# Kernel tuning notes

Measured on AMD Instinct MI355X. Metric: run time of the kernel, lower is better.

## Reference

```python
import jax, jax.numpy as jnp
import numpy as np

N = 50000; E = 800000; T = 800000; G = 64
H = 128; IEMB = 128; BAS = 8; NS = 4; NR = 6; OEH = 128; OUT = 1; NB = 4; CUT = 5.0


def envelope(x):
    # exponent=5 -> p=6: 1/x + a*x^5 + b*x^6 + c*x^7 with a=-28, b=48, c=-21
    return 1.0 / x - 28.0 * x**5 + 48.0 * x**6 - 21.0 * x**7


def setup_inputs() -> dict:
    key = jax.random.key(0)
    ks = iter(jax.random.split(key, 80))
    def w(shape, s=0.1):
        return jax.random.normal(next(ks), shape, dtype=jnp.float32) * s
    inp = {}
    inp['z'] = jax.random.randint(next(ks), (N,), 0, 100, dtype=jnp.int32)
    inp['dist'] = jax.random.uniform(next(ks), (E,), jnp.float32, 0.05, 1.0)
    inp['dist_trip'] = jax.random.uniform(next(ks), (T,), jnp.float32, 0.05, 1.0)
    inp['angle'] = jax.random.uniform(next(ks), (T,), jnp.float32, -1.0, 1.0)
    inp['edge_index'] = jax.random.randint(next(ks), (2, E), 0, N, dtype=jnp.int32)
    inp['triplets'] = jax.random.randint(next(ks), (T, 3), 0, N, dtype=jnp.int32)
    inp['batch'] = jnp.sort(jax.random.randint(next(ks), (N,), 0, G, dtype=jnp.int32))
    inp['atom_table'] = w((100, H), 1.0)
    inp['rbf_freq'] = jnp.arange(1, NR + 1, dtype=jnp.float32) * jnp.float32(np.pi)
    inp['sbf_freq'] = jnp.arange(1, NR + 1, dtype=jnp.float32) * jnp.float32(np.pi)
    inp['emb_w1'] = w((NR, IEMB)); inp['emb_b1'] = w((IEMB,), 0.01)
    inp['emb_w2'] = w((IEMB, H)); inp['emb_b2'] = w((H,), 0.01)
    inp['iw_rbf1'] = w((NB, NR, BAS)); inp['iw_rbf2'] = w((NB, BAS, H))
    inp['iw_sbf1'] = w((NB, NS * NR, BAS)); inp['iw_sbf2'] = w((NB, BAS, IEMB))
    inp['iw_t1'] = w((NB, H, IEMB)); inp['iw_t2'] = w((NB, IEMB, H)); inp['ib_t2'] = w((NB, H), 0.01)
    inp['iw_up'] = w((NB, H, H)); inp['ib_up'] = w((NB, H), 0.01)
    inp['iw_down'] = w((NB, H, H)); inp['ib_down'] = w((NB, H), 0.01)
    inp['ow_rbf'] = w((NB + 1, NR, H))
    inp['ow0'] = w((NB + 1, H, OEH)); inp['ob0'] = w((NB + 1, OEH), 0.01)
    inp['ow1'] = w((NB + 1, OEH, OEH)); inp['ob1'] = w((NB + 1, OEH), 0.01)
    inp['ow2'] = w((NB + 1, OEH, OUT)); inp['ob2'] = w((NB + 1, OUT), 0.01)
    return inp


def _forward(atom_table, rbf_freq, sbf_freq, emb_w1, emb_b1, emb_w2, emb_b2,
             iw_rbf1, iw_rbf2, iw_sbf1, iw_sbf2, iw_t1, iw_t2, ib_t2,
             iw_up, ib_up, iw_down, ib_down, ow_rbf, ow0, ob0, ow1, ob1, ow2, ob2,
             dist, dist_trip, angle, z, edge_index, triplets, batch):
    row, col = edge_index[0], edge_index[1]
    j_idx = triplets[:, 1]
    # radial basis for edges: [E, NR]
    d = dist[:, None] / CUT
    rbf_e = envelope(d) * jnp.sin(rbf_freq * d)
    # spherical basis for triplets: [T, NS*NR]
    dt = dist_trip[:, None] / CUT
    rbf_t = envelope(dt) * jnp.sin(sbf_freq * dt)
    a = angle[:, None]
    sph = jnp.concatenate([jnp.ones_like(a), a, 0.5 * (3 * a**2 - 1), 0.5 * (5 * a**3 - 3 * a)], axis=-1)
    sbf_t = (rbf_t[:, None, :] * sph[:, :, None]).reshape(a.shape[0], -1)

    x = atom_table[z]  # [N, H]
    # EmbeddingBlock: edge msg from rbf only, scattered to col
    e = jax.nn.silu(rbf_e @ emb_w1 + emb_b1) @ emb_w2 + emb_b2
    x = x + jax.ops.segment_sum(e, col, num_segments=N)

    def out_block(k, x):
        rbf_emb = rbf_e @ ow_rbf[k]            # [E, H]
        h = jax.ops.segment_sum(x[row] * rbf_emb, col, num_segments=N)
        h = jax.nn.silu(h @ ow0[k] + ob0[k])
        h = jax.nn.silu(h @ ow1[k] + ob1[k])
        return h @ ow2[k] + ob2[k]             # [N, OUT]

    P = out_block(0, x)
    for b in range(NB):
        x_up = x @ iw_up[b] + ib_up[b]
        x_down = x @ iw_down[b] + ib_down[b]
        rbf_emb = jax.nn.silu(rbf_e @ iw_rbf1[b]) @ iw_rbf2[b]      # [E, H]
        x_edge = x_up[row] * rbf_emb                                  # [E, H]
        sbf_emb = jax.nn.silu(sbf_t @ iw_sbf1[b]) @ iw_sbf2[b]      # [T, H]
        t = jax.nn.silu(x_down @ iw_t1[b]) @ iw_t2[b] + ib_t2[b]     # [N, H]
        # original: for each triplet i, x_edge += t[j]*sbf_emb[i] (broadcast over all edges)
        extra = jnp.sum(t[j_idx] * sbf_emb, axis=0)                   # [H]
        x_edge = x_edge + extra
        x = x + jax.ops.segment_sum(x_edge, col, num_segments=N)
        P = P + out_block(b + 1, x)

    counts = jax.ops.segment_sum(jnp.ones((x.shape[0],), jnp.float32), batch, num_segments=G)
    pooled = jax.ops.segment_sum(P, batch, num_segments=G) / jnp.maximum(counts, 1.0)[:, None]
    return pooled  # [G, OUT]


def reference(z, dist, dist_trip, angle, edge_index, triplets, batch, atom_table, rbf_freq, sbf_freq,
              emb_w1, emb_b1, emb_w2, emb_b2, iw_rbf1, iw_rbf2, iw_sbf1, iw_sbf2, iw_t1, iw_t2, ib_t2,
              iw_up, ib_up, iw_down, ib_down, ow_rbf, ow0, ob0, ow1, ob1, ow2, ob2):
    return _forward(atom_table, rbf_freq, sbf_freq, emb_w1, emb_b1, emb_w2, emb_b2,
                    iw_rbf1, iw_rbf2, iw_sbf1, iw_sbf2, iw_t1, iw_t2, ib_t2,
                    iw_up, ib_up, iw_down, ib_down, ow_rbf, ow0, ob0, ow1, ob1, ow2, ob2,
                    dist, dist_trip, angle, z, edge_index, triplets, batch)
```

## Files before the change

### kernel.cpp

```cpp
#include <hip/hip_runtime.h>
#include <hip/hip_fp16.h>

#define N_ 50000
#define E_ 800000
#define T_ 800000
#define G_ 64
#define H_ 128

#define NBK 782
#define NSB (NBK * 8)
#define CAPS 320

typedef __attribute__((ext_vector_type(8))) short bf16x8;
typedef __attribute__((ext_vector_type(4))) float f32x4;
typedef _Float16 f16x2 __attribute__((ext_vector_type(2)));

__device__ __forceinline__ float siluf(float v) {
    return __fdividef(v, 1.0f + __expf(-v));
}

__device__ __forceinline__ unsigned short f2bf(float f) {
    unsigned int u = __float_as_uint(f);
    u += 0x7fffu + ((u >> 16) & 1u);
    return (unsigned short)(u >> 16);
}
__device__ __forceinline__ unsigned int f2bf2(float a, float b) {
    return (unsigned int)f2bf(a) | ((unsigned int)f2bf(b) << 16);
}
__device__ __forceinline__ float bf2f(unsigned short h) {
    return __uint_as_float(((unsigned int)h) << 16);
}
__device__ __forceinline__ float2 bf2x2(unsigned int p) {
    return make_float2(__uint_as_float(p << 16), __uint_as_float(p & 0xffff0000u));
}
__device__ __forceinline__ float fdot2f(f16x2 a, f16x2 b, float c) {
    return __builtin_amdgcn_fdot2(a, b, c, false);
}

__global__ __launch_bounds__(256) void k_bucket(const int* __restrict__ ecol, const int* __restrict__ erow,
                                                const float* __restrict__ dist,
                                                const int* __restrict__ trip,
                                                const float* __restrict__ dist_trip, const float* __restrict__ angle,
                                                int* bcntE, int4* __restrict__ ebkt,
                                                int* bcntT, int4* __restrict__ tbkt) {
    int i = blockIdx.x * 256 + threadIdx.x;
    int r = blockIdx.x & 7;
    if (i < E_) {
        int col = ecol[i];
        int sb = (col >> 6) * 8 + r;
        int pos = atomicAdd(&bcntE[sb], 1);
        if (pos < CAPS)
            ebkt[(size_t)sb * CAPS + pos] = make_int4(erow[i], __float_as_int(dist[i]), col & 63, 0);
    }
    int t = i - E_;
    if (t >= 0 && t < T_) {
        int j = trip[3 * t + 1];
        int sb = (j >> 6) * 8 + r;
        int pos = atomicAdd(&bcntT[sb], 1);
        if (pos < CAPS)
            tbkt[(size_t)sb * CAPS + pos] = make_int4(__float_as_int(dist_trip[t]), __float_as_int(angle[t]), j & 63, 0);
    }
}

__global__ __launch_bounds__(256) void k_cnt(const int* __restrict__ bcntE, const int4* __restrict__ ebkt,
                                             const int* __restrict__ bcntT, const int4* __restrict__ tbkt,
                                             int* __restrict__ degE, int* __restrict__ degT) {
    int b = blockIdx.x;
    bool isE = b < NBK;
    if (!isE) b -= NBK;
    __shared__ int c[64];
    int tid = threadIdx.x;
    if (tid < 64) c[tid] = 0;
    __syncthreads();
    const int* bcnt = isE ? bcntE : bcntT;
    const int4* bk = isE ? ebkt : tbkt;
    for (int s = 0; s < 8; ++s) {
        int sb = b * 8 + s;
        int nb = min(bcnt[sb], CAPS);
        for (int i = tid; i < nb; i += 256) atomicAdd(&c[bk[(size_t)sb * CAPS + i].z], 1);
    }
    __syncthreads();
    if (tid < 64) {
        int col = b * 64 + tid;
        if (col < N_) (isE ? degE : degT)[col] = c[tid];
    }
}

__global__ __launch_bounds__(1024) void k_scan2(const int* __restrict__ degE, int* rowptrE, int* curE,
                                                const int* __restrict__ degT, int* rowptrT, int* curT, int n) {
    const int* deg = (blockIdx.x == 0) ? degE : degT;
    int* rowptr = (blockIdx.x == 0) ? rowptrE : rowptrT;
    int* cur = (blockIdx.x == 0) ? curE : curT;
    __shared__ int wsum[16];
    __shared__ int s_carry;
    int tid = threadIdx.x, lane = tid & 63, w = tid >> 6;
    if (tid == 0) s_carry = 0;
    __syncthreads();
    for (int base = 0; base < n; base += 1024) {
        int i = base + tid;
        int v = (i < n) ? deg[i] : 0;
        int incl = v;
        #pragma unroll
        for (int s = 1; s < 64; s <<= 1) {
            int t = __shfl_up(incl, (unsigned)s, 64);
            if (lane >= s) incl += t;
        }
        if (lane == 63) wsum[w] = incl;
        __syncthreads();
        int carry0 = s_carry;
        int wexcl = 0;
        for (int j = 0; j < w; ++j) wexcl += wsum[j];
        int excl = carry0 + wexcl + (incl - v);
        if (i < n) { rowptr[i] = excl; cur[i] = excl; }
        __syncthreads();
        if (tid == 1023) s_carry = carry0 + wexcl + incl;
        __syncthreads();
    }
    if (tid == 0) rowptr[n] = s_carry;
}

__global__ __launch_bounds__(256) void k_place(const int* __restrict__ bcntE, const int4* __restrict__ ebkt, int* curE,
                                               int* __restrict__ slist, float* __restrict__ distS,
                                               const int* __restrict__ bcntT, const int4* __restrict__ tbkt, int* curT,
                                               float2* __restrict__ tpay) {
    int b = blockIdx.x;
    bool isE = b < NBK;
    if (!isE) b -= NBK;
    int tid = threadIdx.x;
    if (isE) {
        for (int s = 0; s < 8; ++s) {
            int sb = b * 8 + s;
            int nb = min(bcntE[sb], CAPS);
            for (int i = tid; i < nb; i += 256) {
                int4 pr = ebkt[(size_t)sb * CAPS + i];
                int col = b * 64 + pr.z;
                int pos = atomicAdd(&curE[col], 1);
                slist[pos] = pr.x;
                distS[pos] = __int_as_float(pr.y);
            }
        }
    } else {
        for (int s = 0; s < 8; ++s) {
            int sb = b * 8 + s;
            int nb = min(bcntT[sb], CAPS);
            for (int i = tid; i < nb; i += 256) {
                int4 pr = tbkt[(size_t)sb * CAPS + i];
                int col = b * 64 + pr.z;
                int pos = atomicAdd(&curT[col], 1);
                tpay[pos] = make_float2(__int_as_float(pr.x), __int_as_float(pr.y));
            }
        }
    }
}

__global__ __launch_bounds__(256) void k_wprep(const float* __restrict__ emb_w2, const float* __restrict__ iw_down,
                                               const float* __restrict__ iw_t1, const float* __restrict__ iw_t2,
                                               const float* __restrict__ iw_up, const float* __restrict__ ow0,
                                               const float* __restrict__ ow1, unsigned short* __restrict__ Wt) {
    int mat = blockIdx.x >> 3;
    int part = blockIdx.x & 7;
    const float* src;
    if (mat == 0) src = emb_w2;
    else if (mat < 5) src = iw_down + (size_t)(mat - 1) * 16384;
    else if (mat < 9) src = iw_t1 + (size_t)(mat - 5) * 16384;
    else if (mat < 13) src = iw_t2 + (size_t)(mat - 9) * 16384;
    else if (mat < 17) src = iw_up + (size_t)(mat - 13) * 16384;
    else if (mat < 22) src = ow0 + (size_t)(mat - 17) * 16384;
    else src = ow1 + (size_t)(mat - 22) * 16384;
    unsigned short* dst = Wt + (size_t)mat * 16384;
    int base = part * 2048;
    for (int i = base + threadIdx.x; i < base + 2048; i += 256) {
        int k = i >> 7, n = i & 127;
        dst[n * 128 + k] = f2bf(src[i]);
    }
}

__global__ __launch_bounds__(256) void k_geom(const float* __restrict__ distS,
                                              const float* __restrict__ freq, const float* __restrict__ iw_rbf1,
                                              float* __restrict__ rbfS, __half* __restrict__ s8all, int n) {
    __shared__ float W1s[4][48];
    int tid = threadIdx.x;
    if (tid < 192) W1s[tid / 48][tid % 48] = iw_rbf1[tid];
    __syncthreads();
    int p = blockIdx.x * 256 + tid;
    if (p >= n) return;
    float d = distS[p] * 0.2f;
    float d2 = d * d, d4 = d2 * d2, d5 = d4 * d;
    float env = __fdividef(1.0f, d) - 28.0f * d5 + 48.0f * d5 * d - 21.0f * d5 * d2;
    float rb[6];
    #pragma unroll
    for (int r = 0; r < 6; ++r) {
        rb[r] = env * __sinf(freq[r] * d);
        rbfS[(size_t)p * 6 + r] = rb[r];
    }
    #pragma unroll
    for (int b = 0; b < 4; ++b) {
        __half out[8];
        #pragma unroll
        for (int k = 0; k < 8; ++k) {
            float u = 0.f;
            #pragma unroll
            for (int r = 0; r < 6; ++r) u += rb[r] * W1s[b][r * 8 + k];
            out[k] = __float2half(siluf(u));
        }
        *(uint4*)&s8all[((size_t)b * n + p) * 8] = *(uint4*)out;
    }
}

__global__ __launch_bounds__(256) void k_basis(const float2* __restrict__ tpay,
                                               const float* __restrict__ sfreq, __half* __restrict__ basis, int n) {
    int t = blockIdx.x * 256 + threadIdx.x;
    if (t >= n) return;
    float2 da = tpay[t];
    float d = da.x * 0.2f;
    float a = da.y;
    float d2 = d * d, d4 = d2 * d2, d5 = d4 * d;
    float env = __fdividef(1.0f, d) - 28.0f * d5 + 48.0f * d5 * d - 21.0f * d5 * d2;
    float rb[6];
    #pragma unroll
    for (int r = 0; r < 6; ++r) rb[r] = env * __sinf(sfreq[r] * d);
    float sph[4];
    sph[0] = 1.0f; sph[1] = a; sph[2] = 1.5f * a * a - 0.5f; sph[3] = 2.5f * a * a * a - 1.5f * a;
    __half out[24];
    #pragma unroll
    for (int s = 0; s < 4; ++s)
        #pragma unroll
        for (int r = 0; r < 6; ++r) out[s * 6 + r] = __float2half(sph[s] * rb[r]);
    uint4* dst = (uint4*)(basis + (size_t)t * 24);
    dst[0] = ((uint4*)out)[0];
    dst[1] = ((uint4*)out)[1];
    dst[2] = ((uint4*)out)[2];
}

__global__ __launch_bounds__(256) void k_sv4(const int* __restrict__ rowptrT, const __half* __restrict__ basis,
                                             const float* __restrict__ iw_sbf1, float* __restrict__ SV4, int n) {
    int wave = threadIdx.x >> 6, lane = threadIdx.x & 63;
    int node = blockIdx.x * 8 + wave * 2 + (lane >> 5);
    int sub = lane & 31;
    int blk = sub >> 3, k = sub & 7;
    if (node >= n) return;
    const float* W1 = iw_sbf1 + blk * 192;
    f16x2 w[12];
    #pragma unroll
    for (int j = 0; j < 12; ++j) {
        f16x2 t;
        t.x = (_Float16)W1[(2 * j) * 8 + k];
        t.y = (_Float16)W1[(2 * j + 1) * 8 + k];
        w[j] = t;
    }
    float acc = 0.f;
    int p0 = rowptrT[node], p1 = rowptrT[node + 1];
    for (int p = p0; p < p1; ++p) {
        union { uint4 q[3]; f16x2 h[12]; } bs;
        const uint4* bp = (const uint4*)(basis + (size_t)p * 24);
        bs.q[0] = bp[0]; bs.q[1] = bp[1]; bs.q[2] = bp[2];
        float u = 0.f;
        #pragma unroll
        for (int j = 0; j < 12; ++j) u = fdot2f(bs.h[j], w[j], u);
        acc += siluf(u);
    }
    SV4[((size_t)blk * n + node) * 8 + k] = acc;
}

__global__ __launch_bounds__(256) void k_init_x(const float* __restrict__ atab, const int* __restrict__ z,
                                                unsigned short* __restrict__ xh, int n) {
    int t = blockIdx.x * 256 + threadIdx.x;
    if (t >= n * 16) return;
    int node = t >> 4, q = t & 15;
    const float4* a4 = (const float4*)atab;
    float4 v0 = a4[(size_t)z[node] * 32 + q * 2];
    float4 v1 = a4[(size_t)z[node] * 32 + q * 2 + 1];
    uint4 pk;
    pk.x = f2bf2(v0.x, v0.y);
    pk.y = f2bf2(v0.z, v0.w);
    pk.z = f2bf2(v1.x, v1.y);
    pk.w = f2bf2(v1.z, v1.w);
    ((uint4*)xh)[t] = pk;
}

__global__ __launch_bounds__(256) void k_embS(const int* __restrict__ rowptr, const float* __restrict__ rbfS,
                                              const float* __restrict__ w1, const float* __restrict__ b1,
                                              float* __restrict__ SS, int n) {
    int node = blockIdx.x * 4 + (threadIdx.x >> 6);
    int lane = threadIdx.x & 63;
    if (node >= n) return;
    int c = lane * 2;
    float wc0[6], wc1[6];
    #pragma unroll
    for (int r = 0; r < 6; ++r) { wc0[r] = w1[r * 128 + c]; wc1[r] = w1[r * 128 + c + 1]; }
    float bb0 = b1[c], bb1 = b1[c + 1];
    float a0 = 0.f, a1 = 0.f;
    int p0 = rowptr[node], p1 = rowptr[node + 1];
    for (int p = p0; p < p1; ++p) {
        const float2* r2 = (const float2*)&rbfS[(size_t)p * 6];
        float2 ra = r2[0], rbx = r2[1], rc = r2[2];
        float u0 = bb0 + ra.x * wc0[0] + ra.y * wc0[1] + rbx.x * wc0[2] + rbx.y * wc0[3] + rc.x * wc0[4] + rc.y * wc0[5];
        float u1 = bb1 + ra.x * wc1[0] + ra.y * wc1[1] + rbx.x * wc1[2] + rbx.y * wc1[3] + rc.x * wc1[4] + rc.y * wc1[5];
        a0 += siluf(u0);
        a1 += siluf(u1);
    }
    SS[node * 128 + c] = a0;
    SS[node * 128 + c + 1] = a1;
}

template <int BIAS_MODE, bool SILU, bool ACCBF, bool ABF, bool WF32, bool WBF>
__global__ __launch_bounds__(256, 4) void k_gemm_mfma(const void* __restrict__ Ap,
                                                      const unsigned short* __restrict__ Wt,
                                                      const float* __restrict__ bias, const int* __restrict__ deg,
                                                      float* __restrict__ C, unsigned short* __restrict__ Ch, int M) {
    int tid = threadIdx.x;
    int wave = tid >> 6, lane = tid & 63;
    int m15 = lane & 15, quad = lane >> 4;
    int row0 = blockIdx.x * 64 + wave * 16;
    int arow = row0 + m15;
    if (arow > M - 1) arow = M - 1;

    f32x4 acc[8];
    #pragma unroll
    for (int nt = 0; nt < 8; ++nt) acc[nt] = (f32x4){0.f, 0.f, 0.f, 0.f};

    #pragma unroll
    for (int kt = 0; kt < 4; ++kt) {
        int ks = kt * 32 + quad * 8;
        bf16x8 av;
        if constexpr (ABF) {
            av = *(const bf16x8*)((const unsigned short*)Ap + (size_t)arow * 128 + ks);
        } else {
            const float* Arow = (const float*)Ap + (size_t)arow * 128;
            float4 a0 = *(const float4*)(Arow + ks);
            float4 a1 = *(const float4*)(Arow + ks + 4);
            union { bf16x8 v; unsigned int u[4]; } af;
            af.u[0] = f2bf2(a0.x, a0.y);
            af.u[1] = f2bf2(a0.z, a0.w);
            af.u[2] = f2bf2(a1.x, a1.y);
            af.u[3] = f2bf2(a1.z, a1.w);
            av = af.v;
        }
        #pragma unroll
        for (int nt = 0; nt < 8; ++nt) {
            bf16x8 bf = *(const bf16x8*)(Wt + (size_t)(nt * 16 + m15) * 128 + ks);
            acc[nt] = __builtin_amdgcn_mfma_f32_16x16x32_bf16(av, bf, acc[nt], 0, 0, 0);
        }
    }

    #pragma unroll
    for (int nt = 0; nt < 8; ++nt) {
        int col = nt * 16 + m15;
        float bc = 0.f;
        if constexpr (BIAS_MODE != 0) bc = bias[col];
        #pragma unroll
        for (int reg = 0; reg < 4; ++reg) {
            int row = row0 + quad * 4 + reg;
            if (row < M) {
                float v = acc[nt][reg];
                if constexpr (BIAS_MODE == 1) v += bc;
                if constexpr (BIAS_MODE == 2) v += bc * (float)deg[row];
                if constexpr (SILU) v = siluf(v);
                if constexpr (ACCBF) v += bf2f(Ch[(size_t)row * 128 + col]);
                if constexpr (WF32) C[(size_t)row * 128 + col] = v;
                if constexpr (WBF) Ch[(size_t)row * 128 + col] = f2bf(v);
            }
        }
    }
}

template <int PACC>
__global__ __launch_bounds__(256, 4) void k_out_mlp(const unsigned short* __restrict__ hB,
                                                    const unsigned short* __restrict__ W0t, const float* __restrict__ b0,
                                                    const unsigned short* __restrict__ W1t, const float* __restrict__ b1,
                                                    const float* __restrict__ w2col, const float* __restrict__ ob2p,
                                                    float* __restrict__ Pout, int M) {
    __shared__ unsigned short lds[4][16 * 136];
    int tid = threadIdx.x;
    int wave = tid >> 6, lane = tid & 63;
    int m15 = lane & 15, quad = lane >> 4;
    int row0 = blockIdx.x * 64 + wave * 16;
    int arow = row0 + m15;
    if (arow > M - 1) arow = M - 1;
    unsigned short* L = lds[wave];

    f32x4 acc[8];
    #pragma unroll
    for (int nt = 0; nt < 8; ++nt) acc[nt] = (f32x4){0.f, 0.f, 0.f, 0.f};
    #pragma unroll
    for (int kt = 0; kt < 4; ++kt) {
        int ks = kt * 32 + quad * 8;
        bf16x8 av = *(const bf16x8*)(hB + (size_t)arow * 128 + ks);
        #pragma unroll
        for (int nt = 0; nt < 8; ++nt) {
            bf16x8 bf = *(const bf16x8*)(W0t + (size_t)(nt * 16 + m15) * 128 + ks);
            acc[nt] = __builtin_amdgcn_mfma_f32_16x16x32_bf16(av, bf, acc[nt], 0, 0, 0);
        }
    }
    #pragma unroll
    for (int nt = 0; nt < 8; ++nt) {
        int col = nt * 16 + m15;
        float bc = b0[col];
        #pragma unroll
        for (int reg = 0; reg < 4; ++reg)
            L[(quad * 4 + reg) * 136 + col] = f2bf(siluf(acc[nt][reg] + bc));
    }
    __syncthreads();

    #pragma unroll
    for (int nt = 0; nt < 8; ++nt) acc[nt] = (f32x4){0.f, 0.f, 0.f, 0.f};
    #pragma unroll
    for (int kt = 0; kt < 4; ++kt) {
        int ks = kt * 32 + quad * 8;
        bf16x8 av = *(const bf16x8*)(L + m15 * 136 + ks);
        #pragma unroll
        for (int nt = 0; nt < 8; ++nt) {
            bf16x8 bf = *(const bf16x8*)(W1t + (size_t)(nt * 16 + m15) * 128 + ks);
            acc[nt] = __builtin_amdgcn_mfma_f32_16x16x32_bf16(av, bf, acc[nt], 0, 0, 0);
        }
    }
    float w2c[8], pp[4];
    #pragma unroll
    for (int nt = 0; nt < 8; ++nt) w2c[nt] = w2col[nt * 16 + m15];
    #pragma unroll
    for (int reg = 0; reg < 4; ++reg) pp[reg] = 0.f;
    #pragma unroll
    for (int nt = 0; nt < 8; ++nt) {
        float bc = b1[nt * 16 + m15];
        #pragma unroll
        for (int reg = 0; reg < 4; ++reg)
            pp[reg] += siluf(acc[nt][reg] + bc) * w2c[nt];
    }
    #pragma unroll
    for (int reg = 0; reg < 4; ++reg) {
        float s = pp[reg];
        s += __shfl_xor(s, 1, 64);
        s += __shfl_xor(s, 2, 64);
        s += __shfl_xor(s, 4, 64);
        s += __shfl_xor(s, 8, 64);
        if (m15 == 0) {
            int row = row0 + quad * 4 + reg;
            if (row < M) {
                float r = s + ob2p[0];
                if constexpr (PACC == 2) r += Pout[row];
                Pout[row] = r;
            }
        }
    }
}

__global__ __launch_bounds__(256, 4) void k_block_mlp(const unsigned short* __restrict__ xh,
                                                      const unsigned short* __restrict__ Wd, const float* __restrict__ bd,
                                                      const unsigned short* __restrict__ Wt1,
                                                      const unsigned short* __restrict__ Wt2, const float* __restrict__ bt2,
                                                      const unsigned short* __restrict__ Wup, const float* __restrict__ bup,
                                                      float* __restrict__ Tm, unsigned short* __restrict__ xuph, int M) {
    __shared__ unsigned short lds[4][16 * 136];
    int tid = threadIdx.x;
    int wave = tid >> 6, lane = tid & 63;
    int m15 = lane & 15, quad = lane >> 4;
    int row0 = blockIdx.x * 64 + wave * 16;
    int arow = row0 + m15;
    if (arow > M - 1) arow = M - 1;
    unsigned short* L = lds[wave];

    f32x4 accD[8], accU[8];
    #pragma unroll
    for (int nt = 0; nt < 8; ++nt) { accD[nt] = (f32x4){0.f, 0.f, 0.f, 0.f}; accU[nt] = (f32x4){0.f, 0.f, 0.f, 0.f}; }
    #pragma unroll
    for (int kt = 0; kt < 4; ++kt) {
        int ks = kt * 32 + quad * 8;
        bf16x8 av = *(const bf16x8*)(xh + (size_t)arow * 128 + ks);
        #pragma unroll
        for (int nt = 0; nt < 8; ++nt) {
            bf16x8 bd_ = *(const bf16x8*)(Wd + (size_t)(nt * 16 + m15) * 128 + ks);
            accD[nt] = __builtin_amdgcn_mfma_f32_16x16x32_bf16(av, bd_, accD[nt], 0, 0, 0);
            bf16x8 bu_ = *(const bf16x8*)(Wup + (size_t)(nt * 16 + m15) * 128 + ks);
            accU[nt] = __builtin_amdgcn_mfma_f32_16x16x32_bf16(av, bu_, accU[nt], 0, 0, 0);
        }
    }
    #pragma unroll
    for (int nt = 0; nt < 8; ++nt) {
        int col = nt * 16 + m15;
        float bcu = bup[col], bcd = bd[col];
        #pragma unroll
        for (int reg = 0; reg < 4; ++reg) {
            int row = row0 + quad * 4 + reg;
            if (row < M) xuph[(size_t)row * 128 + col] = f2bf(accU[nt][reg] + bcu);
            L[(quad * 4 + reg) * 136 + col] = f2bf(accD[nt][reg] + bcd);
        }
    }
    __syncthreads();

    #pragma unroll
    for (int nt = 0; nt < 8; ++nt) accD[nt] = (f32x4){0.f, 0.f, 0.f, 0.f};
    #pragma unroll
    for (int kt = 0; kt < 4; ++kt) {
        int ks = kt * 32 + quad * 8;
        bf16x8 av = *(const bf16x8*)(L + m15 * 136 + ks);
        #pragma unroll
        for (int nt = 0; nt < 8; ++nt) {
            bf16x8 bf = *(const bf16x8*)(Wt1 + (size_t)(nt * 16 + m15) * 128 + ks);
            accD[nt] = __builtin_amdgcn_mfma_f32_16x16x32_bf16(av, bf, accD[nt], 0, 0, 0);
        }
    }
    __syncthreads();
    #pragma unroll
    for (int nt = 0; nt < 8; ++nt) {
        int col = nt * 16 + m15;
        #pragma unroll
        for (int reg = 0; reg < 4; ++reg)
            L[(quad * 4 + reg) * 136 + col] = f2bf(siluf(accD[nt][reg]));
    }
    __syncthreads();

    #pragma unroll
    for (int nt = 0; nt < 8; ++nt) accD[nt] = (f32x4){0.f, 0.f, 0.f, 0.f};
    #pragma unroll
    for (int kt = 0; kt < 4; ++kt) {
        int ks = kt * 32 + quad * 8;
        bf16x8 av = *(const bf16x8*)(L + m15 * 136 + ks);
        #pragma unroll
        for (int nt = 0; nt < 8; ++nt) {
            bf16x8 bf = *(const bf16x8*)(Wt2 + (size_t)(nt * 16 + m15) * 128 + ks);
            accD[nt] = __builtin_amdgcn_mfma_f32_16x16x32_bf16(av, bf, accD[nt], 0, 0, 0);
        }
    }
    #pragma unroll
    for (int nt = 0; nt < 8; ++nt) {
        int col = nt * 16 + m15;
        float bc = bt2[col];
        #pragma unroll
        for (int reg = 0; reg < 4; ++reg) {
            int row = row0 + quad * 4 + reg;
            if (row < M) Tm[(size_t)row * 128 + col] = accD[nt][reg] + bc;
        }
    }
}

__global__ __launch_bounds__(256) void k_out_gather(const int* __restrict__ rowptr, const int* __restrict__ slist,
                                                    const float* __restrict__ rbfS,
                                                    const unsigned short* __restrict__ xh,
                                                    const float* __restrict__ wrbf,
                                                    unsigned short* __restrict__ hB, int n) {
    int node = blockIdx.x * 4 + (threadIdx.x >> 6);
    int lane = threadIdx.x & 63;
    if (node >= n) return;
    int c = lane * 2;
    float wc0[6], wc1[6];
    #pragma unroll
    for (int r = 0; r < 6; ++r) { wc0[r] = wrbf[r * 128 + c]; wc1[r] = wrbf[r * 128 + c + 1]; }
    float a0 = 0.f, a1 = 0.f;
    int p0 = rowptr[node], p1 = rowptr[node + 1];
    int p = p0;
    for (; p + 4 <= p1; p += 4) {
        int s0 = slist[p], s1 = slist[p + 1], s2 = slist[p + 2], s3 = slist[p + 3];
        float2 rb[4][3];
        #pragma unroll
        for (int u = 0; u < 4; ++u) {
            const float2* r2 = (const float2*)&rbfS[(size_t)(p + u) * 6];
            rb[u][0] = r2[0]; rb[u][1] = r2[1]; rb[u][2] = r2[2];
        }
        unsigned int xv0 = *(const unsigned int*)&xh[(size_t)s0 * 128 + c];
        unsigned int xv1 = *(const unsigned int*)&xh[(size_t)s1 * 128 + c];
        unsigned int xv2 = *(const unsigned int*)&xh[(size_t)s2 * 128 + c];
        unsigned int xv3 = *(const unsigned int*)&xh[(size_t)s3 * 128 + c];
        #pragma unroll
        for (int u = 0; u < 4; ++u) {
            float e0 = rb[u][0].x * wc0[0] + rb[u][0].y * wc0[1] + rb[u][1].x * wc0[2] +
                       rb[u][1].y * wc0[3] + rb[u][2].x * wc0[4] + rb[u][2].y * wc0[5];
            float e1 = rb[u][0].x * wc1[0] + rb[u][0].y * wc1[1] + rb[u][1].x * wc1[2] +
                       rb[u][1].y * wc1[3] + rb[u][2].x * wc1[4] + rb[u][2].y * wc1[5];
            float2 xf = bf2x2((u == 0) ? xv0 : (u == 1) ? xv1 : (u == 2) ? xv2 : xv3);
            a0 += xf.x * e0;
            a1 += xf.y * e1;
        }
    }
    for (; p < p1; ++p) {
        int src = slist[p];
        const float2* r2 = (const float2*)&rbfS[(size_t)p * 6];
        float2 ra = r2[0], rbx = r2[1], rc = r2[2];
        float e0 = ra.x * wc0[0] + ra.y * wc0[1] + rbx.x * wc0[2] + rbx.y * wc0[3] + rc.x * wc0[4] + rc.y * wc0[5];
        float e1 = ra.x * wc1[0] + ra.y * wc1[1] + rbx.x * wc1[2] + rbx.y * wc1[3] + rc.x * wc1[4] + rc.y * wc1[5];
        float2 xf = bf2x2(*(const unsigned int*)&xh[(size_t)src * 128 + c]);
        a0 += xf.x * e0;
        a1 += xf.y * e1;
    }
    *(unsigned int*)&hB[(size_t)node * 128 + c] = f2bf2(a0, a1);
}

__global__ __launch_bounds__(256) void k_extra_fused(const float* __restrict__ Tm, const float* __restrict__ SV,
                                                     const float* __restrict__ W2, float* __restrict__ extra, int n) {
    int tid = threadIdx.x;
    int c = tid & 127, half = tid >> 7;
    float acc[8];
    #pragma unroll
    for (int k = 0; k < 8; ++k) acc[k] = 0.f;
    for (int nn = blockIdx.x * 2 + half; nn < n; nn += gridDim.x * 2) {
        const float4* sv4 = (const float4*)&SV[(size_t)nn * 8];
        float4 s0 = sv4[0], s1 = sv4[1];
        float t = Tm[(size_t)nn * 128 + c];
        acc[0] += t * s0.x; acc[1] += t * s0.y; acc[2] += t * s0.z; acc[3] += t * s0.w;
        acc[4] += t * s1.x; acc[5] += t * s1.y; acc[6] += t * s1.z; acc[7] += t * s1.w;
    }
    float e = 0.f;
    #pragma unroll
    for (int k = 0; k < 8; ++k) e += acc[k] * W2[k * 128 + c];
    __shared__ float red[256];
    red[tid] = e;
    __syncthreads();
    if (tid < 128) atomicAdd(&extra[c], red[tid] + red[tid + 128]);
}

__global__ __launch_bounds__(256) void k_interact(const int* __restrict__ rowptr, const int* __restrict__ slist,
                                                  const __half* __restrict__ s8, const float* __restrict__ W2,
                                                  const float* __restrict__ extra,
                                                  const unsigned short* __restrict__ xuph,
                                                  unsigned short* __restrict__ xh, int n) {
    int node = blockIdx.x * 4 + (threadIdx.x >> 6);
    int lane = threadIdx.x & 63;
    if (node >= n) return;
    int c = lane * 2;
    f16x2 w2a[4], w2b[4];
    #pragma unroll
    for (int j = 0; j < 4; ++j) {
        f16x2 wa, wb;
        wa.x = (_Float16)W2[(2 * j) * 128 + c];
        wa.y = (_Float16)W2[(2 * j + 1) * 128 + c];
        wb.x = (_Float16)W2[(2 * j) * 128 + c + 1];
        wb.y = (_Float16)W2[(2 * j + 1) * 128 + c + 1];
        w2a[j] = wa;
        w2b[j] = wb;
    }
    int p0 = rowptr[node], p1 = rowptr[node + 1];
    float cntf = (float)(p1 - p0);
    float a0 = cntf * extra[c], a1 = cntf * extra[c + 1];
    int p = p0;
    for (; p + 4 <= p1; p += 4) {
        int s0 = slist[p], s1 = slist[p + 1], s2 = slist[p + 2], s3 = slist[p + 3];
        uint4 sv[4];
        #pragma unroll
        for (int u = 0; u < 4; ++u) sv[u] = *(const uint4*)(s8 + (size_t)(p + u) * 8);
        unsigned int xv0 = *(const unsigned int*)&xuph[(size_t)s0 * 128 + c];
        unsigned int xv1 = *(const unsigned int*)&xuph[(size_t)s1 * 128 + c];
        unsigned int xv2 = *(const unsigned int*)&xuph[(size_t)s2 * 128 + c];
        unsigned int xv3 = *(const unsigned int*)&xuph[(size_t)s3 * 128 + c];
        #pragma unroll
        for (int u = 0; u < 4; ++u) {
            union { uint4 q; f16x2 h[4]; } s;
            s.q = sv[u];
            float e0 = fdot2f(s.h[0], w2a[0], 0.f);
            e0 = fdot2f(s.h[1], w2a[1], e0);
            e0 = fdot2f(s.h[2], w2a[2], e0);
            e0 = fdot2f(s.h[3], w2a[3], e0);
            float e1 = fdot2f(s.h[0], w2b[0], 0.f);
            e1 = fdot2f(s.h[1], w2b[1], e1);
            e1 = fdot2f(s.h[2], w2b[2], e1);
            e1 = fdot2f(s.h[3], w2b[3], e1);
            float2 xf = bf2x2((u == 0) ? xv0 : (u == 1) ? xv1 : (u == 2) ? xv2 : xv3);
            a0 += xf.x * e0;
            a1 += xf.y * e1;
        }
    }
    for (; p < p1; ++p) {
        int src = slist[p];
        float2 xf = bf2x2(*(const unsigned int*)&xuph[(size_t)src * 128 + c]);
        union { uint4 q; f16x2 h[4]; } s;
        s.q = *(const uint4*)(s8 + (size_t)p * 8);
        float e0 = fdot2f(s.h[0], w2a[0], 0.f);
        e0 = fdot2f(s.h[1], w2a[1], e0);
        e0 = fdot2f(s.h[2], w2a[2], e0);
        e0 = fdot2f(s.h[3], w2a[3], e0);
        float e1 = fdot2f(s.h[0], w2b[0], 0.f);
        e1 = fdot2f(s.h[1], w2b[1], e1);
        e1 = fdot2f(s.h[2], w2b[2], e1);
        e1 = fdot2f(s.h[3], w2b[3], e1);
        a0 += xf.x * e0;
        a1 += xf.y * e1;
    }
    unsigned int cur = *(unsigned int*)&xh[(size_t)node * 128 + c];
    float2 xc = bf2x2(cur);
    *(unsigned int*)&xh[(size_t)node * 128 + c] = f2bf2(xc.x + a0, xc.y + a1);
}

__global__ __launch_bounds__(256) void k_pool(const float* __restrict__ P, const int* __restrict__ batch,
                                              float* __restrict__ pool, float* __restrict__ cnt, int n) {
    int i = blockIdx.x * 256 + threadIdx.x;
    int lane = threadIdx.x & 63;
    int b = (i < n) ? batch[i] : -1;
    float p = (i < n) ? P[i] : 0.f;
    int b0 = __shfl(b, 0, 64);
    int b63 = __shfl(b, 63, 64);
    if (b0 == b63 && b0 >= 0) {
        float s = p;
        #pragma unroll
        for (int off = 32; off > 0; off >>= 1) s += __shfl_xor(s, off, 64);
        if (lane == 0) {
            atomicAdd(&pool[b0], s);
            atomicAdd(&cnt[b0], 64.0f);
        }
    } else {
        if (i < n) {
            atomicAdd(&pool[b], p);
            atomicAdd(&cnt[b], 1.0f);
        }
    }
}

__global__ __launch_bounds__(64) void k_final(const float* __restrict__ pool, const float* __restrict__ cnt,
                                              float* __restrict__ out) {
    int g = threadIdx.x;
    if (g < G_) out[g] = __fdividef(pool[g], fmaxf(cnt[g], 1.0f));
}

extern "C" void kernel_launch(void* const* d_in, const int* in_sizes, int n_in,
                              void* d_out, int out_size, void* d_ws, size_t ws_size,
                              hipStream_t stream) {
    (void)in_sizes; (void)n_in; (void)out_size; (void)ws_size;
    const int* z = (const int*)d_in[0];
    const float* dist = (const float*)d_in[1];
    const float* dist_trip = (const float*)d_in[2];
    const float* angle = (const float*)d_in[3];
    const int* edge_index = (const int*)d_in[4];
    const int* triplets = (const int*)d_in[5];
    const int* batch = (const int*)d_in[6];
    const float* atom_table = (const float*)d_in[7];
    const float* rbf_freq = (const float*)d_in[8];
    const float* sbf_freq = (const float*)d_in[9];
    const float* emb_w1 = (const float*)d_in[10];
    const float* emb_b1 = (const float*)d_in[11];
    const float* emb_w2 = (const float*)d_in[12];
    const float* emb_b2 = (const float*)d_in[13];
    const float* iw_rbf1 = (const float*)d_in[14];
    const float* iw_rbf2 = (const float*)d_in[15];
    const float* iw_sbf1 = (const float*)d_in[16];
    const float* iw_sbf2 = (const float*)d_in[17];
    const float* iw_t1 = (const float*)d_in[18];
    const float* iw_t2 = (const float*)d_in[19];
    const float* ib_t2 = (const float*)d_in[20];
    const float* iw_up = (const float*)d_in[21];
    const float* ib_up = (const float*)d_in[22];
    const float* iw_down = (const float*)d_in[23];
    const float* ib_down = (const float*)d_in[24];
    const float* ow_rbf = (const float*)d_in[25];
    const float* ow0 = (const float*)d_in[26];
    const float* ob0 = (const float*)d_in[27];
    const float* ow1 = (const float*)d_in[28];
    const float* ob1 = (const float*)d_in[29];
    const float* ow2 = (const float*)d_in[30];
    const float* ob2 = (const float*)d_in[31];

    const int* erow = edge_index;
    const int* ecol = edge_index + E_;

    float* ws = (float*)d_ws;
    float* bufA = ws;
    float* bufB = bufA + (size_t)N_ * H_;
    float* P = bufB + (size_t)N_ * H_;
    float* rbfS = P + N_;
    float* SV4 = rbfS + (size_t)E_ * 6;
    float* extra4 = SV4 + (size_t)4 * N_ * 8;
    float* pool = extra4 + 512;
    float* cnt = pool + G_;
    int* bcntE = (int*)(cnt + G_);
    int* bcntT = bcntE + NSB;
    int* degE = bcntT + NSB;
    int* degT = degE + N_;
    int* rowptr = degT + N_;
    int* curE = rowptr + N_ + 1;
    int* curT = curE + N_;
    int* slist = curT + N_;
    int* rowptrT = slist + E_;
    float* distS = (float*)(rowptrT + N_ + 1);
    uintptr_t tp = (uintptr_t)(distS + E_);
    tp = (tp + 7) & ~(uintptr_t)7;
    float2* tpay = (float2*)tp;
    __half* s8all = (__half*)(tpay + T_);
    __half* basis = s8all + (size_t)4 * E_ * 8;
    unsigned short* xh = (unsigned short*)(basis + (size_t)T_ * 24);
    unsigned short* xuph = xh + (size_t)N_ * H_;
    unsigned short* Wt = xuph + (size_t)N_ * H_;
    unsigned short* hB = (unsigned short*)bufB;

    int4* ebkt = (int4*)s8all;
    int4* tbkt = ebkt + (size_t)NSB * CAPS;

    const int EG = (E_ + 255) / 256;
    const int TG = (T_ + 255) / 256;
    const int ETG = (E_ + T_ + 255) / 256;
    const int NG4 = (N_ + 3) / 4;
    const int GEMMG = (N_ + 63) / 64;

    hipMemsetAsync(extra4, 0, (512 + 2 * G_ + 2 * NSB) * sizeof(float), stream);
    k_wprep<<<27 * 8, 256, 0, stream>>>(emb_w2, iw_down, iw_t1, iw_t2, iw_up, ow0, ow1, Wt);
    k_bucket<<<ETG, 256, 0, stream>>>(ecol, erow, dist, triplets, dist_trip, angle,
                                      bcntE, ebkt, bcntT, tbkt);
    k_cnt<<<2 * NBK, 256, 0, stream>>>(bcntE, ebkt, bcntT, tbkt, degE, degT);
    k_scan2<<<2, 1024, 0, stream>>>(degE, rowptr, curE, degT, rowptrT, curT, N_);
    k_place<<<2 * NBK, 256, 0, stream>>>(bcntE, ebkt, curE, slist, distS,
                                         bcntT, tbkt, curT, tpay);

    k_geom<<<EG, 256, 0, stream>>>(distS, rbf_freq, iw_rbf1, rbfS, s8all, E_);
    k_basis<<<TG, 256, 0, stream>>>(tpay, sbf_freq, basis, T_);
    k_sv4<<<(N_ + 7) / 8, 256, 0, stream>>>(rowptrT, basis, iw_sbf1, SV4, N_);
    k_init_x<<<(N_ * 16 + 255) / 256, 256, 0, stream>>>(atom_table, z, xh, N_);

    k_embS<<<NG4, 256, 0, stream>>>(rowptr, rbfS, emb_w1, emb_b1, bufA, N_);
    k_gemm_mfma<2, false, true, false, false, true><<<GEMMG, 256, 0, stream>>>(
        bufA, Wt, emb_b2, degE, nullptr, xh, N_);

    auto out_block = [&](int k, bool first) {
        k_out_gather<<<NG4, 256, 0, stream>>>(rowptr, slist, rbfS, xh,
                                              ow_rbf + (size_t)k * 6 * 128, hB, N_);
        if (first)
            k_out_mlp<1><<<GEMMG, 256, 0, stream>>>(hB, Wt + (size_t)(17 + k) * 16384, ob0 + k * 128,
                                                    Wt + (size_t)(22 + k) * 16384, ob1 + k * 128,
                                                    ow2 + k * 128, ob2 + k, P, N_);
        else
            k_out_mlp<2><<<GEMMG, 256, 0, stream>>>(hB, Wt + (size_t)(17 + k) * 16384, ob0 + k * 128,
                                                    Wt + (size_t)(22 + k) * 16384, ob1 + k * 128,
                                                    ow2 + k * 128, ob2 + k, P, N_);
    };

    out_block(0, true);

    for (int b = 0; b < 4; ++b) {
        k_block_mlp<<<GEMMG, 256, 0, stream>>>(xh,
                                               Wt + (size_t)(1 + b) * 16384, ib_down + b * 128,
                                               Wt + (size_t)(5 + b) * 16384,
                                               Wt + (size_t)(9 + b) * 16384, ib_t2 + b * 128,
                                               Wt + (size_t)(13 + b) * 16384, ib_up + b * 128,
                                               bufA, xuph, N_);
        k_extra_fused<<<256, 256, 0, stream>>>(bufA, SV4 + (size_t)b * N_ * 8,
                                               iw_sbf2 + (size_t)b * 1024, extra4 + b * 128, N_);
        k_interact<<<NG4, 256, 0, stream>>>(rowptr, slist, s8all + (size_t)b * E_ * 8,
                                            iw_rbf2 + (size_t)b * 1024, extra4 + b * 128,
                                            xuph, xh, N_);
        out_block(b + 1, false);
    }

    k_pool<<<(N_ + 255) / 256, 256, 0, stream>>>(P, batch, pool, cnt, N_);
    k_final<<<1, 64, 0, stream>>>(pool, cnt, (float*)d_out);
}
```

Measured before the change: 1.705 ms.

## Fuse triplet extra reduction into block MLP epilogue and store embedding sums as bf16

The block MLP kernel now reduces its T output directly against the per-node SV vectors and the sbf projection weights. It accumulates the per-column extra vector in shared memory and adds it to global memory with one atomic per column per block. This removes the fp32 Tm write and the separate k_extra_fused pass, at the cost of extra LDS use and more FMAs in the epilogue. Separately, the embedding sums are written as packed bf16 and consumed by the GEMM through its bf16-A path, which halves that traffic but loses some precision.

```diff
diff --git a/kernel.cpp b/kernel.cpp
--- a/kernel.cpp
+++ b/kernel.cpp
@@ -280,7 +280,7 @@
 
 __global__ __launch_bounds__(256) void k_embS(const int* __restrict__ rowptr, const float* __restrict__ rbfS,
                                               const float* __restrict__ w1, const float* __restrict__ b1,
-                                              float* __restrict__ SS, int n) {
+                                              unsigned short* __restrict__ SS, int n) {
     int node = blockIdx.x * 4 + (threadIdx.x >> 6);
     int lane = threadIdx.x & 63;
     if (node >= n) return;
@@ -299,8 +299,7 @@
         a0 += siluf(u0);
         a1 += siluf(u1);
     }
-    SS[node * 128 + c] = a0;
-    SS[node * 128 + c + 1] = a1;
+    *(unsigned int*)&SS[(size_t)node * 128 + c] = f2bf2(a0, a1);
 }
 
 template <int BIAS_MODE, bool SILU, bool ACCBF, bool ABF, bool WF32, bool WBF>
@@ -449,8 +448,12 @@
                                                       const unsigned short* __restrict__ Wt1,
                                                       const unsigned short* __restrict__ Wt2, const float* __restrict__ bt2,
                                                       const unsigned short* __restrict__ Wup, const float* __restrict__ bup,
-                                                      float* __restrict__ Tm, unsigned short* __restrict__ xuph, int M) {
+                                                      const float* __restrict__ SVb, const float* __restrict__ W2ex,
+                                                      float* __restrict__ extra,
+                                                      unsigned short* __restrict__ xuph, int M) {
     __shared__ unsigned short lds[4][16 * 136];
+    __shared__ float W2s[1024];
+    __shared__ float exs[128];
     int tid = threadIdx.x;
     int wave = tid >> 6, lane = tid & 63;
     int m15 = lane & 15, quad = lane >> 4;
@@ -458,6 +461,9 @@
     int arow = row0 + m15;
     if (arow > M - 1) arow = M - 1;
     unsigned short* L = lds[wave];
+    #pragma unroll
+    for (int i = 0; i < 4; ++i) W2s[tid + i * 256] = W2ex[tid + i * 256];
+    if (tid < 128) exs[tid] = 0.f;
 
     f32x4 accD[8], accU[8];
     #pragma unroll
@@ -521,16 +527,41 @@
             accD[nt] = __builtin_amdgcn_mfma_f32_16x16x32_bf16(av, bf, accD[nt], 0, 0, 0);
         }
     }
+    float epart[8];
+    #pragma unroll
+    for (int nt = 0; nt < 8; ++nt) epart[nt] = 0.f;
+    #pragma unroll
+    for (int reg = 0; reg < 4; ++reg) {
+        int row = row0 + quad * 4 + reg;
+        float sv[8];
+        if (row < M) {
+            const float4* s4 = (const float4*)&SVb[(size_t)row * 8];
+            float4 v0 = s4[0], v1 = s4[1];
+            sv[0] = v0.x; sv[1] = v0.y; sv[2] = v0.z; sv[3] = v0.w;
+            sv[4] = v1.x; sv[5] = v1.y; sv[6] = v1.z; sv[7] = v1.w;
+        } else {
+            #pragma unroll
+            for (int k = 0; k < 8; ++k) sv[k] = 0.f;
+        }
+        #pragma unroll
+        for (int nt = 0; nt < 8; ++nt) {
+            int col = nt * 16 + m15;
+            float tm = accD[nt][reg] + bt2[col];
+            float d = 0.f;
+            #pragma unroll
+            for (int k = 0; k < 8; ++k) d += sv[k] * W2s[k * 128 + col];
+            epart[nt] += tm * d;
+        }
+    }
     #pragma unroll
     for (int nt = 0; nt < 8; ++nt) {
-        int col = nt * 16 + m15;
-        float bc = bt2[col];
-        #pragma unroll
-        for (int reg = 0; reg < 4; ++reg) {
-            int row = row0 + quad * 4 + reg;
-            if (row < M) Tm[(size_t)row * 128 + col] = accD[nt][reg] + bc;
-        }
-    }
+        float s = epart[nt];
+        s += __shfl_xor(s, 16, 64);
+        s += __shfl_xor(s, 32, 64);
+        if (quad == 0) atomicAdd(&exs[nt * 16 + m15], s);
+    }
+    __syncthreads();
+    if (tid < 128) atomicAdd(&extra[tid], exs[tid]);
 }
 
 __global__ __launch_bounds__(256) void k_out_gather(const int* __restrict__ rowptr, const int* __restrict__ slist,
@@ -582,29 +613,6 @@
         a1 += xf.y * e1;
     }
     *(unsigned int*)&hB[(size_t)node * 128 + c] = f2bf2(a0, a1);
-}
-
-__global__ __launch_bounds__(256) void k_extra_fused(const float* __restrict__ Tm, const float* __restrict__ SV,
-                                                     const float* __restrict__ W2, float* __restrict__ extra, int n) {
-    int tid = threadIdx.x;
-    int c = tid & 127, half = tid >> 7;
-    float acc[8];
-    #pragma unroll
-    for (int k = 0; k < 8; ++k) acc[k] = 0.f;
-    for (int nn = blockIdx.x * 2 + half; nn < n; nn += gridDim.x * 2) {
-        const float4* sv4 = (const float4*)&SV[(size_t)nn * 8];
-        float4 s0 = sv4[0], s1 = sv4[1];
-        float t = Tm[(size_t)nn * 128 + c];
-        acc[0] += t * s0.x; acc[1] += t * s0.y; acc[2] += t * s0.z; acc[3] += t * s0.w;
-        acc[4] += t * s1.x; acc[5] += t * s1.y; acc[6] += t * s1.z; acc[7] += t * s1.w;
-    }
-    float e = 0.f;
-    #pragma unroll
-    for (int k = 0; k < 8; ++k) e += acc[k] * W2[k * 128 + c];
-    __shared__ float red[256];
-    red[tid] = e;
-    __syncthreads();
-    if (tid < 128) atomicAdd(&extra[c], red[tid] + red[tid + 128]);
 }
 
 __global__ __launch_bounds__(256) void k_interact(const int* __restrict__ rowptr, const int* __restrict__ slist,
@@ -776,6 +784,7 @@
     unsigned short* xuph = xh + (size_t)N_ * H_;
     unsigned short* Wt = xuph + (size_t)N_ * H_;
     unsigned short* hB = (unsigned short*)bufB;
+    unsigned short* SSb = (unsigned short*)bufA;
 
     int4* ebkt = (int4*)s8all;
     int4* tbkt = ebkt + (size_t)NSB * CAPS;
@@ -800,9 +809,9 @@
     k_sv4<<<(N_ + 7) / 8, 256, 0, stream>>>(rowptrT, basis, iw_sbf1, SV4, N_);
     k_init_x<<<(N_ * 16 + 255) / 256, 256, 0, stream>>>(atom_table, z, xh, N_);
 
-    k_embS<<<NG4, 256, 0, stream>>>(rowptr, rbfS, emb_w1, emb_b1, bufA, N_);
-    k_gemm_mfma<2, false, true, false, false, true><<<GEMMG, 256, 0, stream>>>(
-        bufA, Wt, emb_b2, degE, nullptr, xh, N_);
+    k_embS<<<NG4, 256, 0, stream>>>(rowptr, rbfS, emb_w1, emb_b1, SSb, N_);
+    k_gemm_mfma<2, false, true, true, false, true><<<GEMMG, 256, 0, stream>>>(
+        SSb, Wt, emb_b2, degE, nullptr, xh, N_);
 
     auto out_block = [&](int k, bool first) {
         k_out_gather<<<NG4, 256, 0, stream>>>(rowptr, slist, rbfS, xh,
@@ -825,9 +834,8 @@
                                                Wt + (size_t)(5 + b) * 16384,
                                                Wt + (size_t)(9 + b) * 16384, ib_t2 + b * 128,
                                                Wt + (size_t)(13 + b) * 16384, ib_up + b * 128,
-                                               bufA, xuph, N_);
-        k_extra_fused<<<256, 256, 0, stream>>>(bufA, SV4 + (size_t)b * N_ * 8,
-                                               iw_sbf2 + (size_t)b * 1024, extra4 + b * 128, N_);
+                                               SV4 + (size_t)b * N_ * 8, iw_sbf2 + (size_t)b * 1024,
+                                               extra4 + b * 128, xuph, N_);
         k_interact<<<NG4, 256, 0, stream>>>(rowptr, slist, s8all + (size_t)b * E_ * 8,
                                             iw_rbf2 + (size_t)b * 1024, extra4 + b * 128,
                                             xuph, xh, N_);
```

New measurement: 1.945 ms. 14.1% more time.
